# Optimization experiments

Measured on AMD Instinct MI355X. Metric: run time of the kernel, lower is better.

## Reference

```python
import math
import jax, jax.numpy as jnp
import numpy as np

T, D, H = 2048, 2048, 16
C = D // H
EPS = 1e-6


def _rope_tables(c, t):
    inv_freq = 1.0 / (10000.0 ** (jnp.arange(0, c, 2, dtype=jnp.float32) / c))
    freqs = jnp.arange(t, dtype=jnp.float32)[:, None] * inv_freq[None, :]  # (T, C/2)
    return jnp.sin(freqs), jnp.cos(freqs)


def _rotate_every_two(x):
    x1 = x[..., ::2]
    x2 = x[..., 1::2]
    return jnp.stack((-x2, x1), axis=-1).reshape(x.shape)


def _apply_rope(x_htc, sin, cos):
    # sin/cos: (T, C/2) -> repeat each freq twice along channel -> (1, T, C)
    sin = jnp.repeat(sin, 2, axis=-1)[None]
    cos = jnp.repeat(cos, 2, axis=-1)[None]
    return x_htc * cos + _rotate_every_two(x_htc) * sin


def _layernorm(x, w):
    mu = jnp.mean(x, axis=-1, keepdims=True)
    var = jnp.var(x, axis=-1, keepdims=True)
    return (x - mu) / jnp.sqrt(var + EPS) * w


def setup_inputs() -> dict:
    key = jax.random.key(0)
    ks = jax.random.split(key, 4)
    x = jax.random.normal(ks[0], (T, D), dtype=jnp.float32)
    W_attn = jax.random.normal(ks[1], (3 * D, D), dtype=jnp.float32) * 0.02
    b_attn = jnp.zeros((3 * D,), dtype=jnp.float32)
    W_proj = jax.random.normal(ks[2], (D, D), dtype=jnp.float32) * 0.02
    b_proj = jnp.zeros((D,), dtype=jnp.float32)
    q_ln_w = jnp.ones((C,), dtype=jnp.float32)
    k_ln_w = jnp.ones((C,), dtype=jnp.float32)
    return {"x": x, "W_attn": W_attn, "b_attn": b_attn, "W_proj": W_proj,
            "b_proj": b_proj, "q_ln_w": q_ln_w, "k_ln_w": k_ln_w}


def reference(x, W_attn, b_attn, W_proj, b_proj, q_ln_w, k_ln_w):
    t, d = x.shape
    qkv = x @ W_attn.T + b_attn                      # (T, 3D)
    q, k, v = jnp.split(qkv, 3, axis=-1)
    q = q.reshape(t, H, C).transpose(1, 0, 2)        # (H, T, C)
    k = k.reshape(t, H, C).transpose(1, 0, 2)
    v = v.reshape(t, H, C).transpose(1, 0, 2)
    q = _layernorm(q, q_ln_w)
    k = _layernorm(k, k_ln_w)
    sin, cos = _rope_tables(C, t)
    q = _apply_rope(q, sin, cos)
    k = _apply_rope(k, sin, cos)
    a = jnp.einsum("htc,hsc->hts", q, k)             # (H, T, T)
    causal = jnp.tril(jnp.ones((1, t, t))) == 0
    a = jnp.where(causal, float("-inf"), a)
    scaling = math.sqrt(C)                            # q_ln active
    a = jax.nn.softmax(a.astype(jnp.float32) / scaling, axis=-1).astype(x.dtype)
    out = jnp.einsum("hts,hsc->htc", a, v)           # (H, T, C)
    out = out.transpose(1, 0, 2).reshape(t, d)       # (T, D)
    return out @ W_proj.T + b_proj
```

## Files before the change

kernel.cpp:

```cpp
#include <hip/hip_runtime.h>
#include <hip/hip_bf16.h>
#include <math.h>

#define T_DIM 2048
#define D_DIM 2048
#define H_DIM 16
#define C_DIM 128

typedef __bf16 bf16;
typedef __attribute__((ext_vector_type(8))) __bf16 bf16x8;
typedef __attribute__((ext_vector_type(4))) __bf16 bf16x4;
typedef __attribute__((ext_vector_type(2))) __bf16 bf16x2;
typedef __attribute__((ext_vector_type(4))) float f32x4;

__device__ __forceinline__ void gload_lds16(const void* g, void* l) {
  __builtin_amdgcn_global_load_lds((__attribute__((address_space(1))) void*)g,
                                   (__attribute__((address_space(3))) void*)l,
                                   16, 0, 0);
}

__global__ __launch_bounds__(256) void cvt_f32_to_bf16(
    const float* __restrict__ src, bf16* __restrict__ dst, int n4)
{
  int i = blockIdx.x * blockDim.x + threadIdx.x;
  int stride = gridDim.x * blockDim.x;
  for (; i < n4; i += stride) {
    float4 v = reinterpret_cast<const float4*>(src)[i];
    bf16x4 o;
    o[0] = (bf16)v.x; o[1] = (bf16)v.y; o[2] = (bf16)v.z; o[3] = (bf16)v.w;
    reinterpret_cast<bf16x4*>(dst)[i] = o;
  }
}

__global__ __launch_bounds__(512, 2) void gemm256_bt_bias(
    const bf16* __restrict__ A, const bf16* __restrict__ B,
    const float* __restrict__ bias, float* __restrict__ C,
    int M, int N, int K)
{
  __shared__ __align__(16) bf16 Asl[2][256 * 64];
  __shared__ __align__(16) bf16 Bsl[2][256 * 64];
  const int tid = threadIdx.x;
  const int lane = tid & 63;
  const int wv = tid >> 6;
  const int g = lane >> 4, r16 = lane & 15;

  int bid = blockIdx.x;
  int bid2 = (bid & 7) * (gridDim.x >> 3) + (bid >> 3);
  const int ntn = N >> 8;
  const int bn = bid2 % ntn, bm = bid2 / ntn;

  const size_t Abase = (size_t)(bm * 256) * K;
  const size_t Bbase = (size_t)(bn * 256) * K;

  f32x4 acc[2][2][2][4] = {};
  bf16x8 a[2][2], b[4][2];

  auto stageA = [&](int bb, int ha, int t) {
#pragma unroll
    for (int i = 0; i < 2; ++i) {
      int c = i * 512 + tid;
      int r = c >> 3, p = c & 7, j = p ^ (r & 7);
      gload_lds16(A + Abase + (size_t)(ha * 128 + r) * K + t * 64 + j * 8,
                  (char*)&Asl[bb][0] + ha * 16384 + (size_t)c * 16);
    }
  };
  auto stageB = [&](int bb, int hb, int t) {
#pragma unroll
    for (int i = 0; i < 2; ++i) {
      int c = i * 512 + tid;
      int r = c >> 3, p = c & 7, j = p ^ (r & 7);
      gload_lds16(B + Bbase + (size_t)(hb * 128 + r) * K + t * 64 + j * 8,
                  (char*)&Bsl[bb][0] + hb * 16384 + (size_t)c * 16);
    }
  };
  auto readA = [&](int bufi, int QR) {
#pragma unroll
    for (int R = 0; R < 2; ++R) {
      int ar = QR * 128 + (wv >> 1) * 32 + R * 16 + r16;
#pragma unroll
      for (int ks = 0; ks < 2; ++ks)
        a[R][ks] = *reinterpret_cast<const bf16x8*>(
            &Asl[bufi][ar * 64 + (((ks * 4 + g) ^ (ar & 7)) << 3)]);
    }
  };
  auto readB = [&](int bufi, int QC) {
#pragma unroll
    for (int F = 0; F < 4; ++F) {
      int br = QC * 128 + (wv & 1) * 64 + F * 16 + r16;
#pragma unroll
      for (int ks = 0; ks < 2; ++ks)
        b[F][ks] = *reinterpret_cast<const bf16x8*>(
            &Bsl[bufi][br * 64 + (((ks * 4 + g) ^ (br & 7)) << 3)]);
    }
  };
  auto mfma16 = [&](f32x4 (&c2)[2][4]) {
    __builtin_amdgcn_s_setprio(1);
#pragma unroll
    for (int ks = 0; ks < 2; ++ks)
#pragma unroll
      for (int R = 0; R < 2; ++R)
#pragma unroll
        for (int F = 0; F < 4; ++F)
          c2[R][F] = __builtin_amdgcn_mfma_f32_16x16x32_bf16(a[R][ks], b[F][ks], c2[R][F], 0, 0, 0);
    __builtin_amdgcn_s_setprio(0);
  };

#define MIDSYNC(VM)                                               \
  asm volatile("s_waitcnt vmcnt(" #VM ")" ::: "memory");          \
  __builtin_amdgcn_s_barrier();                                   \
  asm volatile("s_waitcnt lgkmcnt(0)" ::: "memory");              \
  __builtin_amdgcn_sched_barrier(0);

  stageA(0, 0, 0); stageB(0, 0, 0); stageB(0, 1, 0); stageA(0, 1, 0);
  asm volatile("s_waitcnt vmcnt(4)" ::: "memory");
  __builtin_amdgcn_s_barrier();

  const int NT = K >> 6;
  for (int t = 0; t < NT; ++t) {
    const int cb = t & 1, nb = cb ^ 1;
    const bool pf = (t + 1 < NT);
    readA(cb, 0);
    readB(cb, 0);
    if (pf) stageA(nb, 0, t + 1);
    MIDSYNC(4)
    mfma16(acc[0][0]);
    __builtin_amdgcn_s_barrier();
    readB(cb, 1);
    if (pf) stageB(nb, 0, t + 1);
    MIDSYNC(4)
    mfma16(acc[0][1]);
    __builtin_amdgcn_s_barrier();
    readA(cb, 1);
    if (pf) stageB(nb, 1, t + 1);
    __builtin_amdgcn_s_barrier();
    asm volatile("s_waitcnt lgkmcnt(0)" ::: "memory");
    __builtin_amdgcn_sched_barrier(0);
    mfma16(acc[1][1]);
    __builtin_amdgcn_s_barrier();
    readB(cb, 0);
    if (pf) stageA(nb, 1, t + 1);
    MIDSYNC(4)
    mfma16(acc[1][0]);
    __builtin_amdgcn_s_barrier();
  }
#undef MIDSYNC

#pragma unroll
  for (int qr = 0; qr < 2; ++qr)
#pragma unroll
    for (int qc = 0; qc < 2; ++qc)
#pragma unroll
      for (int R = 0; R < 2; ++R)
#pragma unroll
        for (int F = 0; F < 4; ++F) {
          int row0 = bm * 256 + qr * 128 + (wv >> 1) * 32 + R * 16 + g * 4;
          int col  = bn * 256 + qc * 128 + (wv & 1) * 64 + F * 16 + r16;
          float bv = bias[col];
#pragma unroll
          for (int rr = 0; rr < 4; ++rr)
            C[(size_t)(row0 + rr) * N + col] = acc[qr][qc][R][F][rr] + bv;
        }
}

__global__ __launch_bounds__(256) void gemm_bt_bias(
    const bf16* __restrict__ A, const bf16* __restrict__ B,
    const float* __restrict__ bias, float* __restrict__ C,
    int M, int N, int K)
{
  __shared__ __align__(16) bf16 As[2][128 * 32];
  __shared__ __align__(16) bf16 Bs[2][128 * 32];
  const int tid = threadIdx.x;
  const int lane = tid & 63;
  const int w = tid >> 6;
  const int wm = (w >> 1) * 64, wn = (w & 1) * 64;
  const int g = lane >> 4;
  const int r16 = lane & 15;
  const int bm = blockIdx.y, bn = blockIdx.x;

  f32x4 acc[4][4] = {};

  const size_t Abase = (size_t)(bm * 128) * K;
  const size_t Bbase = (size_t)(bn * 128) * K;

  auto stage = [&](int bb, int k0) {
#pragma unroll
    for (int c = 0; c < 2; ++c) {
      int e = c * 256 + tid;
      int row = e >> 2, col = (e & 3) * 8;
      gload_lds16(A + Abase + (size_t)row * K + k0 + col, (char*)&As[bb][0] + (size_t)e * 16);
      gload_lds16(B + Bbase + (size_t)row * K + k0 + col, (char*)&Bs[bb][0] + (size_t)e * 16);
    }
  };

  stage(0, 0);
  __syncthreads();

  for (int k0 = 0; k0 < K; k0 += 32) {
    const int cur = (k0 >> 5) & 1;
    if (k0 + 32 < K) stage(cur ^ 1, k0 + 32);
    bf16x8 a[4], b[4];
#pragma unroll
    for (int m = 0; m < 4; ++m)
      a[m] = *reinterpret_cast<const bf16x8*>(&As[cur][(wm + m * 16 + r16) * 32 + g * 8]);
#pragma unroll
    for (int n = 0; n < 4; ++n)
      b[n] = *reinterpret_cast<const bf16x8*>(&Bs[cur][(wn + n * 16 + r16) * 32 + g * 8]);
    __builtin_amdgcn_s_setprio(1);
#pragma unroll
    for (int m = 0; m < 4; ++m)
#pragma unroll
      for (int n = 0; n < 4; ++n)
        acc[m][n] = __builtin_amdgcn_mfma_f32_16x16x32_bf16(a[m], b[n], acc[m][n], 0, 0, 0);
    __builtin_amdgcn_s_setprio(0);
    __syncthreads();
  }

#pragma unroll
  for (int m = 0; m < 4; ++m) {
    int row0 = bm * 128 + wm + m * 16 + g * 4;
#pragma unroll
    for (int n = 0; n < 4; ++n) {
      int col = bn * 128 + wn + n * 16 + r16;
      float bv = bias[col];
#pragma unroll
      for (int rr = 0; rr < 4; ++rr)
        C[(size_t)(row0 + rr) * N + col] = acc[m][n][rr] + bv;
    }
  }
}

__global__ __launch_bounds__(256) void ln_rope_kernel(
    const float* __restrict__ qkv, const float* __restrict__ qw,
    const float* __restrict__ kw, bf16* __restrict__ qo, bf16* __restrict__ ko)
{
  const int tid = threadIdx.x;
  const int lane = tid & 63;
  const int wid = blockIdx.x * 4 + (tid >> 6);
  const int h = wid >> 11;
  const int t = wid & (T_DIM - 1);
  const int c0 = lane * 2;

  float inv_freq = exp2f(-13.287712379549449f * (float)c0 * (1.0f / 128.0f));
  float fr = (float)t * inv_freq;
  float sn = sinf(fr), cs = cosf(fr);
  const float scaleq = 0.08838834764831845f;

#pragma unroll
  for (int which = 0; which < 2; ++which) {
    const float* base = qkv + (size_t)t * (3 * D_DIM) + which * D_DIM + h * C_DIM;
    float2 v = *reinterpret_cast<const float2*>(base + c0);
    float s = v.x + v.y;
#pragma unroll
    for (int m = 32; m; m >>= 1) s += __shfl_xor(s, m);
    float mu = s * (1.0f / 128.0f);
    float d0 = v.x - mu, d1 = v.y - mu;
    float ss = d0 * d0 + d1 * d1;
#pragma unroll
    for (int m = 32; m; m >>= 1) ss += __shfl_xor(ss, m);
    float rstd = rsqrtf(ss * (1.0f / 128.0f) + 1e-6f);
    const float* wgt = which ? kw : qw;
    float x0 = d0 * rstd * wgt[c0], x1 = d1 * rstd * wgt[c0 + 1];
    float o0 = x0 * cs - x1 * sn;
    float o1 = x1 * cs + x0 * sn;
    if (!which) { o0 *= scaleq; o1 *= scaleq; }
    bf16* out = (which ? ko : qo) + ((size_t)h * T_DIM + t) * C_DIM + c0;
    bf16x2 ob; ob[0] = (bf16)o0; ob[1] = (bf16)o1;
    *reinterpret_cast<bf16x2*>(out) = ob;
  }
}

__global__ __launch_bounds__(256) void v_transpose_kernel(
    const float* __restrict__ qkv, bf16* __restrict__ vt)
{
  __shared__ bf16 tile[32][33];
  const int h = blockIdx.z;
  const int t0 = blockIdx.x * 32, c0 = blockIdx.y * 32;
  const int tx = threadIdx.x, ty = threadIdx.y;
#pragma unroll
  for (int i = 0; i < 4; ++i) {
    int t = t0 + ty + i * 8;
    tile[ty + i * 8][tx] =
        (bf16)qkv[(size_t)t * (3 * D_DIM) + 2 * D_DIM + h * C_DIM + c0 + tx];
  }
  __syncthreads();
#pragma unroll
  for (int i = 0; i < 4; ++i) {
    int c = c0 + ty + i * 8;
    vt[((size_t)h * C_DIM + c) * T_DIM + t0 + tx] = tile[tx][ty + i * 8];
  }
}

__global__ __launch_bounds__(256, 4) void attn_kernel(
    const bf16* __restrict__ Q, const bf16* __restrict__ K,
    const bf16* __restrict__ VT, bf16* __restrict__ AO,
    float* __restrict__ U, float* __restrict__ ML)
{
  __shared__ __align__(16) bf16 Ks[2][32 * 128];
  __shared__ __align__(16) bf16 Vs[2][128 * 32];
  __shared__ __align__(16) bf16 p_lds[4][16 * 32];
  const int tid = threadIdx.x;
  const int lane = tid & 63;
  const int w = tid >> 6;
  const int g = lane >> 4, r16 = lane & 15;
  const int h = blockIdx.y;
  const int b = blockIdx.x;

  int qb, kb0, kb1, sp;
  if (b < 32) { qb = 16 + (b >> 1); sp = b & 1; kb0 = sp * 32; kb1 = sp ? (2 * qb + 2) : 32; }
  else        { qb = 47 - b;        sp = -1;    kb0 = 0;       kb1 = 2 * qb + 2; }
  const int qr0 = qb * 64 + w * 16;
  const int qrow = qr0 + r16;

  const bf16* Qh = Q + (size_t)h * T_DIM * C_DIM;
  const bf16* Kh = K + (size_t)h * T_DIM * C_DIM;
  const bf16* Vh = VT + (size_t)h * C_DIM * T_DIM;

  bf16x8 qf[4];
#pragma unroll
  for (int kk = 0; kk < 4; ++kk)
    qf[kk] = *reinterpret_cast<const bf16x8*>(
        &Qh[(size_t)qrow * C_DIM + kk * 32 + g * 8]);

  float mrow = -INFINITY, lrow = 0.f;
  f32x4 o[8] = {};

  auto stage = [&](int bb, int kb) {
    const bf16* Kt = Kh + (size_t)(kb * 32) * C_DIM;
    const bf16* Vt = Vh + kb * 32;
#pragma unroll
    for (int i = 0; i < 2; ++i) {
      int e = i * 256 + tid;
      int r = e >> 4, p = e & 15, j = p ^ (r & 7);
      gload_lds16(Kt + r * C_DIM + j * 8, (char*)&Ks[bb][0] + (size_t)e * 16);
    }
#pragma unroll
    for (int i = 0; i < 2; ++i) {
      int e = i * 256 + tid;
      int r = e >> 2, p = e & 3, j = p ^ ((r >> 1) & 3);
      gload_lds16(Vt + (size_t)r * T_DIM + j * 8, (char*)&Vs[bb][0] + (size_t)e * 16);
    }
  };

  stage(0, kb0);
  __syncthreads();
  int buf = 0;

  for (int kb = kb0; kb < kb1; ++kb) {
    if (kb + 1 < kb1) stage(buf ^ 1, kb + 1);

    f32x4 sacc[2] = {};
    __builtin_amdgcn_s_setprio(1);
#pragma unroll
    for (int n = 0; n < 2; ++n) {
      int kr = n * 16 + r16;
      const bf16* kbase = &Ks[buf][kr << 7];
#pragma unroll
      for (int kk = 0; kk < 4; ++kk) {
        bf16x8 kf = *reinterpret_cast<const bf16x8*>(
            kbase + (((kk * 4 + g) ^ (kr & 7)) << 3));
        sacc[n] = __builtin_amdgcn_mfma_f32_16x16x32_bf16(kf, qf[kk], sacc[n], 0, 0, 0);
      }
    }
    __builtin_amdgcn_s_setprio(0);
    if (kb * 32 + 31 > qr0) {
#pragma unroll
      for (int n = 0; n < 2; ++n)
#pragma unroll
        for (int rr = 0; rr < 4; ++rr)
          if (kb * 32 + n * 16 + g * 4 + rr > qrow) sacc[n][rr] = -3.0e38f;
    }
    float mx = fmaxf(fmaxf(fmaxf(sacc[0][0], sacc[0][1]), fmaxf(sacc[0][2], sacc[0][3])),
                     fmaxf(fmaxf(sacc[1][0], sacc[1][1]), fmaxf(sacc[1][2], sacc[1][3])));
    mx = fmaxf(mx, __shfl_xor(mx, 16));
    mx = fmaxf(mx, __shfl_xor(mx, 32));
    float alpha = 1.0f;
    bool need = __any(mx > mrow + 8.0f);
    if (need) {
      float mnew = fmaxf(mrow, mx);
      alpha = __expf(mrow - mnew);
      mrow = mnew;
    }
    float ps = 0.f;
#pragma unroll
    for (int n = 0; n < 2; ++n)
#pragma unroll
      for (int rr = 0; rr < 4; ++rr) {
        float p = __expf(sacc[n][rr] - mrow);
        sacc[n][rr] = p;
        ps += p;
      }
    ps += __shfl_xor(ps, 16);
    ps += __shfl_xor(ps, 32);
    lrow = lrow * alpha + ps;
    if (need) {
#pragma unroll
      for (int nc = 0; nc < 8; ++nc)
#pragma unroll
        for (int rr = 0; rr < 4; ++rr)
          o[nc][rr] *= alpha;
    }
    {
      bf16* prow = &p_lds[w][r16 << 5];
      const int ssw = (r16 >> 1) & 3;
#pragma unroll
      for (int n = 0; n < 2; ++n) {
        bf16x4 pk;
        pk[0] = (bf16)sacc[n][0]; pk[1] = (bf16)sacc[n][1];
        pk[2] = (bf16)sacc[n][2]; pk[3] = (bf16)sacc[n][3];
        int c8 = 2 * n + (g >> 1);
        *reinterpret_cast<bf16x4*>(prow + (((c8 ^ ssw) << 3) | ((g & 1) << 2))) = pk;
      }
    }
    asm volatile("s_waitcnt lgkmcnt(0)" ::: "memory");
    __builtin_amdgcn_s_setprio(1);
    bf16x8 pf = *reinterpret_cast<const bf16x8*>(
        &p_lds[w][(r16 << 5) + ((g ^ ((r16 >> 1) & 3)) << 3)]);
#pragma unroll
    for (int nc = 0; nc < 8; ++nc) {
      int vr = nc * 16 + r16;
      bf16x8 vf = *reinterpret_cast<const bf16x8*>(
          &Vs[buf][(vr << 5) + ((g ^ ((vr >> 1) & 3)) << 3)]);
      o[nc] = __builtin_amdgcn_mfma_f32_16x16x32_bf16(vf, pf, o[nc], 0, 0, 0);
    }
    __builtin_amdgcn_s_setprio(0);
    __syncthreads();
    buf ^= 1;
  }

  if (sp < 0) {
    float inv = 1.0f / lrow;
    bf16* arow = &AO[(size_t)qrow * D_DIM + h * C_DIM + (g << 2)];
#pragma unroll
    for (int nc = 0; nc < 8; ++nc) {
      bf16x4 ob;
      ob[0] = (bf16)(o[nc][0] * inv); ob[1] = (bf16)(o[nc][1] * inv);
      ob[2] = (bf16)(o[nc][2] * inv); ob[3] = (bf16)(o[nc][3] * inv);
      *reinterpret_cast<bf16x4*>(arow + nc * 16) = ob;
    }
  } else {
    const int qi = qb - 16;
    const size_t ubase = ((size_t)(h * 16 + qi) * 2 + sp) * (64 * 128);
    const size_t mlbase = (size_t)(h * 16 + qi) * 256 + sp * 128;
    const int row = w * 16 + r16;
    float* urow = &U[ubase + (size_t)row * 128 + (g << 2)];
#pragma unroll
    for (int nc = 0; nc < 8; ++nc)
      *reinterpret_cast<f32x4*>(urow + nc * 16) = o[nc];
    if (g == 0) {
      ML[mlbase + row] = mrow;
      ML[mlbase + 64 + row] = lrow;
    }
  }
}

__global__ __launch_bounds__(256) void attn_combine(
    const float* __restrict__ U, const float* __restrict__ ML, bf16* __restrict__ AO)
{
  int idx = blockIdx.x * 256 + threadIdx.x;
  int c4 = (idx & 31) * 4;
  int r = idx >> 5;
  int trow = r & 63;
  int qi = (r >> 6) & 15;
  int h = r >> 10;

  size_t mlbase = (size_t)(h * 16 + qi) * 256;
  float m0 = ML[mlbase + trow],       l0 = ML[mlbase + 64 + trow];
  float m1 = ML[mlbase + 128 + trow], l1 = ML[mlbase + 192 + trow];
  float m = fmaxf(m0, m1);
  float a0 = __expf(m0 - m), a1 = __expf(m1 - m);
  float inv = 1.0f / (l0 * a0 + l1 * a1);

  size_t t0 = ((size_t)(h * 16 + qi) * 2) * (64 * 128) + (size_t)trow * 128 + c4;
  float4 u0 = *reinterpret_cast<const float4*>(U + t0);
  float4 u1 = *reinterpret_cast<const float4*>(U + t0 + 64 * 128);
  int t = 1024 + qi * 64 + trow;
  bf16x4 ob;
  ob[0] = (bf16)((u0.x * a0 + u1.x * a1) * inv);
  ob[1] = (bf16)((u0.y * a0 + u1.y * a1) * inv);
  ob[2] = (bf16)((u0.z * a0 + u1.z * a1) * inv);
  ob[3] = (bf16)((u0.w * a0 + u1.w * a1) * inv);
  *reinterpret_cast<bf16x4*>(&AO[(size_t)t * D_DIM + h * C_DIM + c4]) = ob;
}

extern "C" void kernel_launch(void* const* d_in, const int* in_sizes, int n_in,
                              void* d_out, int out_size, void* d_ws, size_t ws_size,
                              hipStream_t stream)
{
  const float* x      = (const float*)d_in[0];
  const float* W_attn = (const float*)d_in[1];
  const float* b_attn = (const float*)d_in[2];
  const float* W_proj = (const float*)d_in[3];
  const float* b_proj = (const float*)d_in[4];
  const float* q_ln_w = (const float*)d_in[5];
  const float* k_ln_w = (const float*)d_in[6];

  char* ws = (char*)d_ws;
  bf16*  x_bf  = (bf16*)(ws + 0);
  bf16*  wa_bf = (bf16*)(ws + 8388608);
  bf16*  wp_bf = (bf16*)(ws + 33554432);
  float* qkv   = (float*)(ws + 41943040);
  bf16*  q_bf  = (bf16*)(ws + 92274688);
  bf16*  k_bf  = (bf16*)(ws + 100663296);
  bf16*  vt    = (bf16*)(ws + 109051904);
  bf16*  ao    = (bf16*)(ws + 117440512);
  float* U  = (float*)(ws + 41943040);
  float* ML = (float*)(ws + 58720256);

  cvt_f32_to_bf16<<<2048, 256, 0, stream>>>(x,      x_bf,  T_DIM * D_DIM / 4);
  cvt_f32_to_bf16<<<2048, 256, 0, stream>>>(W_attn, wa_bf, 3 * D_DIM * D_DIM / 4);
  cvt_f32_to_bf16<<<2048, 256, 0, stream>>>(W_proj, wp_bf, D_DIM * D_DIM / 4);

  gemm256_bt_bias<<<dim3((T_DIM / 256) * (3 * D_DIM / 256)), dim3(512), 0, stream>>>(
      x_bf, wa_bf, b_attn, qkv, T_DIM, 3 * D_DIM, D_DIM);

  ln_rope_kernel<<<(H_DIM * T_DIM) / 4, 256, 0, stream>>>(qkv, q_ln_w, k_ln_w, q_bf, k_bf);
  v_transpose_kernel<<<dim3(T_DIM / 32, C_DIM / 32, H_DIM), dim3(32, 8), 0, stream>>>(qkv, vt);

  attn_kernel<<<dim3(48, H_DIM), 256, 0, stream>>>(q_bf, k_bf, vt, ao, U, ML);
  attn_combine<<<2048, 256, 0, stream>>>(U, ML, ao);

  gemm_bt_bias<<<dim3(D_DIM / 128, T_DIM / 128), 256, 0, stream>>>(
      ao, wp_bf, b_proj, (float*)d_out, T_DIM, D_DIM, D_DIM);
}
```

Baseline: 202.2 us.

## Retile QKV GEMM to 128x384 blocks and fuse small prep kernels

Result: faster. 191.3 us (-5.4%).

```diff
diff --git a/kernel.cpp b/kernel.cpp
--- a/kernel.cpp
+++ b/kernel.cpp
@@ -19,99 +19,110 @@
                                    16, 0, 0);
 }
 
-__global__ __launch_bounds__(256) void cvt_f32_to_bf16(
-    const float* __restrict__ src, bf16* __restrict__ dst, int n4)
-{
-  int i = blockIdx.x * blockDim.x + threadIdx.x;
-  int stride = gridDim.x * blockDim.x;
-  for (; i < n4; i += stride) {
-    float4 v = reinterpret_cast<const float4*>(src)[i];
+__global__ __launch_bounds__(256) void cvt3(
+    const float* __restrict__ x, const float* __restrict__ wa, const float* __restrict__ wp,
+    bf16* __restrict__ xo, bf16* __restrict__ wao, bf16* __restrict__ wpo)
+{
+  const int NX = 1048576, NA = 3145728;
+  int i = blockIdx.x * 256 + threadIdx.x;
+  for (; i < 5242880; i += 2048 * 256) {
+    const float* s; bf16* d; int off;
+    if (i < NX)            { s = x;  d = xo;  off = i; }
+    else if (i < NX + NA)  { s = wa; d = wao; off = i - NX; }
+    else                   { s = wp; d = wpo; off = i - NX - NA; }
+    float4 v = reinterpret_cast<const float4*>(s)[off];
     bf16x4 o;
     o[0] = (bf16)v.x; o[1] = (bf16)v.y; o[2] = (bf16)v.z; o[3] = (bf16)v.w;
-    reinterpret_cast<bf16x4*>(dst)[i] = o;
-  }
-}
-
-__global__ __launch_bounds__(512, 2) void gemm256_bt_bias(
+    reinterpret_cast<bf16x4*>(d)[off] = o;
+  }
+}
+
+__global__ __launch_bounds__(512, 2) void gemm384_bt_bias(
     const bf16* __restrict__ A, const bf16* __restrict__ B,
     const float* __restrict__ bias, float* __restrict__ C,
     int M, int N, int K)
 {
-  __shared__ __align__(16) bf16 Asl[2][256 * 64];
-  __shared__ __align__(16) bf16 Bsl[2][256 * 64];
+  __shared__ __align__(16) bf16 Asl[2][128 * 64];
+  __shared__ __align__(16) bf16 Bsl[2][384 * 64];
   const int tid = threadIdx.x;
   const int lane = tid & 63;
   const int wv = tid >> 6;
   const int g = lane >> 4, r16 = lane & 15;
+  const int wm4 = wv >> 1;
+  const int wn2 = wv & 1;
 
   int bid = blockIdx.x;
-  int bid2 = (bid & 7) * (gridDim.x >> 3) + (bid >> 3);
-  const int ntn = N >> 8;
+  int bid2 = (bid & 7) * 32 + (bid >> 3);
+  const int ntn = N / 384;
   const int bn = bid2 % ntn, bm = bid2 / ntn;
 
-  const size_t Abase = (size_t)(bm * 256) * K;
-  const size_t Bbase = (size_t)(bn * 256) * K;
-
-  f32x4 acc[2][2][2][4] = {};
-  bf16x8 a[2][2], b[4][2];
-
-  auto stageA = [&](int bb, int ha, int t) {
+  const size_t Abase = (size_t)(bm * 128) * K;
+  const size_t Bbase = (size_t)(bn * 384) * K;
+
+  f32x4 acc[4][2][3] = {};
+  bf16x8 a[2][2], b[3][2];
+
+  auto stageA = [&](int bb, int t) {
 #pragma unroll
     for (int i = 0; i < 2; ++i) {
       int c = i * 512 + tid;
       int r = c >> 3, p = c & 7, j = p ^ (r & 7);
-      gload_lds16(A + Abase + (size_t)(ha * 128 + r) * K + t * 64 + j * 8,
-                  (char*)&Asl[bb][0] + ha * 16384 + (size_t)c * 16);
-    }
-  };
-  auto stageB = [&](int bb, int hb, int t) {
+      gload_lds16(A + Abase + (size_t)r * K + t * 64 + j * 8,
+                  (char*)&Asl[bb][0] + (size_t)c * 16);
+    }
+  };
+  auto stageB = [&](int bb, int u, int t) {
 #pragma unroll
     for (int i = 0; i < 2; ++i) {
       int c = i * 512 + tid;
       int r = c >> 3, p = c & 7, j = p ^ (r & 7);
-      gload_lds16(B + Bbase + (size_t)(hb * 128 + r) * K + t * 64 + j * 8,
-                  (char*)&Bsl[bb][0] + hb * 16384 + (size_t)c * 16);
-    }
-  };
-  auto readA = [&](int bufi, int QR) {
+      gload_lds16(B + Bbase + (size_t)(u * 128 + r) * K + t * 64 + j * 8,
+                  (char*)&Bsl[bb][0] + u * 16384 + (size_t)c * 16);
+    }
+  };
+  auto readA = [&](int bufi) {
 #pragma unroll
     for (int R = 0; R < 2; ++R) {
-      int ar = QR * 128 + (wv >> 1) * 32 + R * 16 + r16;
+      int ar = wm4 * 32 + R * 16 + r16;
 #pragma unroll
       for (int ks = 0; ks < 2; ++ks)
         a[R][ks] = *reinterpret_cast<const bf16x8*>(
             &Asl[bufi][ar * 64 + (((ks * 4 + g) ^ (ar & 7)) << 3)]);
     }
   };
-  auto readB = [&](int bufi, int QC) {
-#pragma unroll
-    for (int F = 0; F < 4; ++F) {
-      int br = QC * 128 + (wv & 1) * 64 + F * 16 + r16;
+  auto readB = [&](int bufi, int q) {
+#pragma unroll
+    for (int F = 0; F < 3; ++F) {
+      int br = q * 96 + wn2 * 48 + F * 16 + r16;
 #pragma unroll
       for (int ks = 0; ks < 2; ++ks)
         b[F][ks] = *reinterpret_cast<const bf16x8*>(
             &Bsl[bufi][br * 64 + (((ks * 4 + g) ^ (br & 7)) << 3)]);
     }
   };
-  auto mfma16 = [&](f32x4 (&c2)[2][4]) {
+  auto mfma12 = [&](f32x4 (&cq)[2][3]) {
     __builtin_amdgcn_s_setprio(1);
 #pragma unroll
     for (int ks = 0; ks < 2; ++ks)
 #pragma unroll
       for (int R = 0; R < 2; ++R)
 #pragma unroll
-        for (int F = 0; F < 4; ++F)
-          c2[R][F] = __builtin_amdgcn_mfma_f32_16x16x32_bf16(a[R][ks], b[F][ks], c2[R][F], 0, 0, 0);
+        for (int F = 0; F < 3; ++F)
+          cq[R][F] = __builtin_amdgcn_mfma_f32_16x16x32_bf16(a[R][ks], b[F][ks], cq[R][F], 0, 0, 0);
     __builtin_amdgcn_s_setprio(0);
   };
 
-#define MIDSYNC(VM)                                               \
+#define VMSYNC(VM)                                                \
   asm volatile("s_waitcnt vmcnt(" #VM ")" ::: "memory");          \
   __builtin_amdgcn_s_barrier();                                   \
   asm volatile("s_waitcnt lgkmcnt(0)" ::: "memory");              \
   __builtin_amdgcn_sched_barrier(0);
-
-  stageA(0, 0, 0); stageB(0, 0, 0); stageB(0, 1, 0); stageA(0, 1, 0);
+#define BARSYNC()                                                 \
+  __builtin_amdgcn_s_barrier();                                   \
+  asm volatile("s_waitcnt lgkmcnt(0)" ::: "memory");              \
+  __builtin_amdgcn_sched_barrier(0);
+
+  stageA(0, 0); stageB(0, 0, 0); stageB(0, 1, 0); stageB(0, 2, 0);
   asm volatile("s_waitcnt vmcnt(4)" ::: "memory");
   __builtin_amdgcn_s_barrier();
 
@@ -119,47 +130,44 @@
   for (int t = 0; t < NT; ++t) {
     const int cb = t & 1, nb = cb ^ 1;
     const bool pf = (t + 1 < NT);
-    readA(cb, 0);
+    readA(cb);
     readB(cb, 0);
-    if (pf) stageA(nb, 0, t + 1);
-    MIDSYNC(4)
-    mfma16(acc[0][0]);
+    if (pf) stageA(nb, t + 1);
+    VMSYNC(4)
+    mfma12(acc[0]);
     __builtin_amdgcn_s_barrier();
     readB(cb, 1);
     if (pf) stageB(nb, 0, t + 1);
-    MIDSYNC(4)
-    mfma16(acc[0][1]);
+    VMSYNC(4)
+    mfma12(acc[1]);
     __builtin_amdgcn_s_barrier();
-    readA(cb, 1);
+    readB(cb, 2);
     if (pf) stageB(nb, 1, t + 1);
+    BARSYNC()
+    mfma12(acc[2]);
     __builtin_amdgcn_s_barrier();
-    asm volatile("s_waitcnt lgkmcnt(0)" ::: "memory");
-    __builtin_amdgcn_sched_barrier(0);
-    mfma16(acc[1][1]);
+    readB(cb, 3);
+    if (pf) stageB(nb, 2, t + 1);
+    VMSYNC(4)
+    mfma12(acc[3]);
     __builtin_amdgcn_s_barrier();
-    readB(cb, 0);
-    if (pf) stageA(nb, 1, t + 1);
-    MIDSYNC(4)
-    mfma16(acc[1][0]);
-    __builtin_amdgcn_s_barrier();
-  }
-#undef MIDSYNC
-
-#pragma unroll
-  for (int qr = 0; qr < 2; ++qr)
-#pragma unroll
-    for (int qc = 0; qc < 2; ++qc)
-#pragma unroll
-      for (int R = 0; R < 2; ++R)
-#pragma unroll
-        for (int F = 0; F < 4; ++F) {
-          int row0 = bm * 256 + qr * 128 + (wv >> 1) * 32 + R * 16 + g * 4;
-          int col  = bn * 256 + qc * 128 + (wv & 1) * 64 + F * 16 + r16;
-          float bv = bias[col];
-#pragma unroll
-          for (int rr = 0; rr < 4; ++rr)
-            C[(size_t)(row0 + rr) * N + col] = acc[qr][qc][R][F][rr] + bv;
-        }
+  }
+#undef VMSYNC
+#undef BARSYNC
+
+#pragma unroll
+  for (int q = 0; q < 4; ++q)
+#pragma unroll
+    for (int R = 0; R < 2; ++R)
+#pragma unroll
+      for (int F = 0; F < 3; ++F) {
+        int row0 = bm * 128 + wm4 * 32 + R * 16 + g * 4;
+        int col  = bn * 384 + q * 96 + wn2 * 48 + F * 16 + r16;
+        float bv = bias[col];
+#pragma unroll
+        for (int rr = 0; rr < 4; ++rr)
+          C[(size_t)(row0 + rr) * N + col] = acc[q][R][F][rr] + bv;
+      }
 }
 
 __global__ __launch_bounds__(256) void gemm_bt_bias(
@@ -229,64 +237,65 @@
   }
 }
 
-__global__ __launch_bounds__(256) void ln_rope_kernel(
+__global__ __launch_bounds__(256) void lnrope_vt_kernel(
     const float* __restrict__ qkv, const float* __restrict__ qw,
-    const float* __restrict__ kw, bf16* __restrict__ qo, bf16* __restrict__ ko)
-{
+    const float* __restrict__ kw, bf16* __restrict__ qo, bf16* __restrict__ ko,
+    bf16* __restrict__ vt)
+{
+  __shared__ bf16 tile[32][33];
   const int tid = threadIdx.x;
-  const int lane = tid & 63;
-  const int wid = blockIdx.x * 4 + (tid >> 6);
-  const int h = wid >> 11;
-  const int t = wid & (T_DIM - 1);
-  const int c0 = lane * 2;
-
-  float inv_freq = exp2f(-13.287712379549449f * (float)c0 * (1.0f / 128.0f));
-  float fr = (float)t * inv_freq;
-  float sn = sinf(fr), cs = cosf(fr);
-  const float scaleq = 0.08838834764831845f;
-
-#pragma unroll
-  for (int which = 0; which < 2; ++which) {
-    const float* base = qkv + (size_t)t * (3 * D_DIM) + which * D_DIM + h * C_DIM;
-    float2 v = *reinterpret_cast<const float2*>(base + c0);
-    float s = v.x + v.y;
-#pragma unroll
-    for (int m = 32; m; m >>= 1) s += __shfl_xor(s, m);
-    float mu = s * (1.0f / 128.0f);
-    float d0 = v.x - mu, d1 = v.y - mu;
-    float ss = d0 * d0 + d1 * d1;
-#pragma unroll
-    for (int m = 32; m; m >>= 1) ss += __shfl_xor(ss, m);
-    float rstd = rsqrtf(ss * (1.0f / 128.0f) + 1e-6f);
-    const float* wgt = which ? kw : qw;
-    float x0 = d0 * rstd * wgt[c0], x1 = d1 * rstd * wgt[c0 + 1];
-    float o0 = x0 * cs - x1 * sn;
-    float o1 = x1 * cs + x0 * sn;
-    if (!which) { o0 *= scaleq; o1 *= scaleq; }
-    bf16* out = (which ? ko : qo) + ((size_t)h * T_DIM + t) * C_DIM + c0;
-    bf16x2 ob; ob[0] = (bf16)o0; ob[1] = (bf16)o1;
-    *reinterpret_cast<bf16x2*>(out) = ob;
-  }
-}
-
-__global__ __launch_bounds__(256) void v_transpose_kernel(
-    const float* __restrict__ qkv, bf16* __restrict__ vt)
-{
-  __shared__ bf16 tile[32][33];
-  const int h = blockIdx.z;
-  const int t0 = blockIdx.x * 32, c0 = blockIdx.y * 32;
-  const int tx = threadIdx.x, ty = threadIdx.y;
-#pragma unroll
-  for (int i = 0; i < 4; ++i) {
-    int t = t0 + ty + i * 8;
-    tile[ty + i * 8][tx] =
-        (bf16)qkv[(size_t)t * (3 * D_DIM) + 2 * D_DIM + h * C_DIM + c0 + tx];
-  }
-  __syncthreads();
-#pragma unroll
-  for (int i = 0; i < 4; ++i) {
-    int c = c0 + ty + i * 8;
-    vt[((size_t)h * C_DIM + c) * T_DIM + t0 + tx] = tile[tx][ty + i * 8];
+  if (blockIdx.x < 8192) {
+    const int lane = tid & 63;
+    const int wid = blockIdx.x * 4 + (tid >> 6);
+    const int h = wid >> 11;
+    const int t = wid & (T_DIM - 1);
+    const int c0 = lane * 2;
+
+    float inv_freq = exp2f(-13.287712379549449f * (float)c0 * (1.0f / 128.0f));
+    float fr = (float)t * inv_freq;
+    float sn = sinf(fr), cs = cosf(fr);
+    const float scaleq = 0.08838834764831845f;
+
+#pragma unroll
+    for (int which = 0; which < 2; ++which) {
+      const float* base = qkv + (size_t)t * (3 * D_DIM) + which * D_DIM + h * C_DIM;
+      float2 v = *reinterpret_cast<const float2*>(base + c0);
+      float s = v.x + v.y;
+#pragma unroll
+      for (int m = 32; m; m >>= 1) s += __shfl_xor(s, m);
+      float mu = s * (1.0f / 128.0f);
+      float d0 = v.x - mu, d1 = v.y - mu;
+      float ss = d0 * d0 + d1 * d1;
+#pragma unroll
+      for (int m = 32; m; m >>= 1) ss += __shfl_xor(ss, m);
+      float rstd = rsqrtf(ss * (1.0f / 128.0f) + 1e-6f);
+      const float* wgt = which ? kw : qw;
+      float x0 = d0 * rstd * wgt[c0], x1 = d1 * rstd * wgt[c0 + 1];
+      float o0 = x0 * cs - x1 * sn;
+      float o1 = x1 * cs + x0 * sn;
+      if (!which) { o0 *= scaleq; o1 *= scaleq; }
+      bf16* out = (which ? ko : qo) + ((size_t)h * T_DIM + t) * C_DIM + c0;
+      bf16x2 ob; ob[0] = (bf16)o0; ob[1] = (bf16)o1;
+      *reinterpret_cast<bf16x2*>(out) = ob;
+    }
+  } else {
+    const int vb = blockIdx.x - 8192;
+    const int t0 = (vb & 63) * 32;
+    const int c0 = ((vb >> 6) & 3) * 32;
+    const int h = vb >> 8;
+    const int tx = tid & 31, ty = tid >> 5;
+#pragma unroll
+    for (int i = 0; i < 4; ++i) {
+      int t = t0 + ty + i * 8;
+      tile[ty + i * 8][tx] =
+          (bf16)qkv[(size_t)t * (3 * D_DIM) + 2 * D_DIM + h * C_DIM + c0 + tx];
+    }
+    __syncthreads();
+#pragma unroll
+    for (int i = 0; i < 4; ++i) {
+      int c = c0 + ty + i * 8;
+      vt[((size_t)h * C_DIM + c) * T_DIM + t0 + tx] = tile[tx][ty + i * 8];
+    }
   }
 }
 
@@ -506,15 +515,12 @@
   float* U  = (float*)(ws + 41943040);
   float* ML = (float*)(ws + 58720256);
 
-  cvt_f32_to_bf16<<<2048, 256, 0, stream>>>(x,      x_bf,  T_DIM * D_DIM / 4);
-  cvt_f32_to_bf16<<<2048, 256, 0, stream>>>(W_attn, wa_bf, 3 * D_DIM * D_DIM / 4);
-  cvt_f32_to_bf16<<<2048, 256, 0, stream>>>(W_proj, wp_bf, D_DIM * D_DIM / 4);
-
-  gemm256_bt_bias<<<dim3((T_DIM / 256) * (3 * D_DIM / 256)), dim3(512), 0, stream>>>(
+  cvt3<<<2048, 256, 0, stream>>>(x, W_attn, W_proj, x_bf, wa_bf, wp_bf);
+
+  gemm384_bt_bias<<<dim3((T_DIM / 128) * (3 * D_DIM / 384)), dim3(512), 0, stream>>>(
       x_bf, wa_bf, b_attn, qkv, T_DIM, 3 * D_DIM, D_DIM);
 
-  ln_rope_kernel<<<(H_DIM * T_DIM) / 4, 256, 0, stream>>>(qkv, q_ln_w, k_ln_w, q_bf, k_bf);
-  v_transpose_kernel<<<dim3(T_DIM / 32, C_DIM / 32, H_DIM), dim3(32, 8), 0, stream>>>(qkv, vt);
+  lnrope_vt_kernel<<<8192 + 4096, 256, 0, stream>>>(qkv, q_ln_w, k_ln_w, q_bf, k_bf, vt);
 
   attn_kernel<<<dim3(48, H_DIM), 256, 0, stream>>>(q_bf, k_bf, vt, ao, U, ML);
   attn_combine<<<2048, 256, 0, stream>>>(U, ML, ao);
```
